# Performance work log

Hardware: AMD Instinct MI355X
Metric: run time of the kernel (lower is better)

The kernel has to match this reference:

```python
import jax, jax.numpy as jnp
import numpy as np
import math

DIM = 384
NH = 6
DH = DIM // NH
B = 2
S = 2048
EPS = 1e-6
LN_EPS = 1e-5


def setup_inputs() -> dict:
    key = jax.random.key(0)
    ks = jax.random.split(key, 8)
    q = jax.random.normal(ks[0], (B, S, DIM), dtype=jnp.float32)
    k = jax.random.normal(ks[1], (B, S, DIM), dtype=jnp.float32)
    v = jax.random.normal(ks[2], (B, S, DIM), dtype=jnp.float32)
    # gate linear params (Linear(3*dim, num_heads)); small random weights to exercise the math
    igate_w = jax.random.normal(ks[3], (NH, 3 * DIM), dtype=jnp.float32) * 0.02
    igate_b = jax.random.normal(ks[4], (NH,), dtype=jnp.float32) * 0.1
    fgate_w = jax.random.normal(ks[5], (NH, 3 * DIM), dtype=jnp.float32) * 0.02
    fgate_b = jnp.linspace(3.0, 6.0, NH, dtype=jnp.float32)
    # MultiHeadLayerNorm residual weight (stored as delta, effective scale = 1 + w)
    outnorm_weight = jax.random.normal(ks[6], (DIM,), dtype=jnp.float32) * 0.02
    return {"q": q, "k": k, "v": v, "igate_w": igate_w, "igate_b": igate_b,
            "fgate_w": fgate_w, "fgate_b": fgate_b, "outnorm_weight": outnorm_weight}


def _mlstm_forward(q, k, v, igate_w, igate_b, fgate_w, fgate_b, outnorm_weight):
    Bq, Sq, _ = q.shape
    gate_in = jnp.concatenate([q, k, v], axis=-1)                       # (B,S,3D)
    ig = gate_in @ igate_w.T + igate_b                                   # (B,S,NH)
    fg = gate_in @ fgate_w.T + fgate_b                                   # (B,S,NH)
    # split heads: (B,NH,S,DH)
    qh = q.reshape(Bq, Sq, NH, DH).transpose(0, 2, 1, 3)
    kh = k.reshape(Bq, Sq, NH, DH).transpose(0, 2, 1, 3)
    vh = v.reshape(Bq, Sq, NH, DH).transpose(0, 2, 1, 3)
    ig = ig.transpose(0, 2, 1)                                           # (B,NH,S)
    fg = fg.transpose(0, 2, 1)                                           # (B,NH,S)

    log_fg = jax.nn.log_sigmoid(fg)                                      # (B,NH,S)
    lfc = jnp.concatenate([jnp.zeros((Bq, NH, 1), dtype=q.dtype),
                           jnp.cumsum(log_fg, axis=-1)], axis=-1)        # (B,NH,S+1)
    # log_fg_matrix[i,j] = cumsum[i] - cumsum[j] (sliced [1:,1:]), masked causal
    diff = lfc[:, :, 1:, None] - lfc[:, :, None, 1:]                     # (B,NH,S,S)
    ltr = jnp.tril(jnp.ones((Sq, Sq), dtype=bool))
    log_fg_mat = jnp.where(ltr, diff, -jnp.inf)
    log_D = log_fg_mat + ig[:, :, None, :]                               # + igate^T
    max_log_D = jnp.max(log_D, axis=-1, keepdims=True)                   # rowwise stabilize
    D = jnp.exp(log_D - max_log_D)
    qk = jnp.einsum('bhsd,bhtd->bhst', qh, kh) / math.sqrt(DH)
    C = qk * D
    normalizer = jnp.maximum(jnp.abs(jnp.sum(C, axis=-1, keepdims=True)),
                             jnp.exp(-max_log_D))
    h = jnp.einsum('bhst,bhtd->bhsd', C / (normalizer + EPS), vh)        # (B,NH,S,DH)

    # MultiHeadLayerNorm == group_norm over each head's DH channels, scale=(1+w)
    mean = jnp.mean(h, axis=-1, keepdims=True)
    var = jnp.var(h, axis=-1, keepdims=True)
    normed = (h - mean) / jnp.sqrt(var + LN_EPS)
    scale = (1.0 + outnorm_weight).reshape(NH, DH)[None, :, None, :]
    out = normed * scale
    return out.transpose(0, 2, 1, 3).reshape(Bq, Sq, DIM)


def reference(q, k, v, igate_w, igate_b, fgate_w, fgate_b, outnorm_weight):
    return _mlstm_forward(q, k, v, igate_w, igate_b, fgate_w, fgate_b, outnorm_weight)
```

## Files before the change

### kernel.cpp

```cpp
#include <hip/hip_runtime.h>
#include <math.h>

#define DIM 384
#define NH 6
#define DH 64
#define B_ 2
#define S_ 2048
#define EPS 1e-6f
#define LN_EPS 1e-5f
#define G3 (3*DIM)
#define LOG2E 1.44269504f
#define KSTR 72
#define VSTR 68
#define NT (S_/64)
#define NSPLIT 8
#define NBH (B_*NH)

typedef __attribute__((ext_vector_type(8))) short bf16x8;
typedef __attribute__((ext_vector_type(4))) short bf16x4;
typedef __attribute__((ext_vector_type(4))) float f32x4;

__device__ __forceinline__ unsigned short f2bf(float f){
    unsigned int u = __float_as_uint(f);
    u += 0x7fff + ((u >> 16) & 1);
    return (unsigned short)(u >> 16);
}
__device__ __forceinline__ float bf2f(unsigned short u){
    return __uint_as_float(((unsigned int)u) << 16);
}

__device__ __forceinline__ float logsig(float x){
    return fminf(x, 0.f) - log1pf(expf(-fabsf(x)));
}

__global__ __launch_bounds__(256) void gates_kernel(
    const float* __restrict__ q, const float* __restrict__ k, const float* __restrict__ v,
    const float* __restrict__ iw, const float* __restrict__ ib,
    const float* __restrict__ fw, const float* __restrict__ fb,
    float* __restrict__ ig_out, float* __restrict__ lf_out) {
    int wave = (blockIdx.x * 256 + threadIdx.x) >> 6;
    int lane = threadIdx.x & 63;
    int b = wave / S_, s = wave % S_;
    size_t base = ((size_t)b * S_ + s) * DIM;
    float aI[NH], aF[NH];
    #pragma unroll
    for (int h = 0; h < NH; h++){ aI[h] = 0.f; aF[h] = 0.f; }
    for (int g = lane; g < G3/4; g += 64) {
        int e = g * 4;
        float4 x4;
        if (e < DIM)        x4 = *(const float4*)(q + base + e);
        else if (e < 2*DIM) x4 = *(const float4*)(k + base + e - DIM);
        else                x4 = *(const float4*)(v + base + e - 2*DIM);
        #pragma unroll
        for (int h = 0; h < NH; h++){
            float4 wi = *(const float4*)(iw + h*G3 + e);
            float4 wf = *(const float4*)(fw + h*G3 + e);
            aI[h] = fmaf(x4.x, wi.x, fmaf(x4.y, wi.y, fmaf(x4.z, wi.z, fmaf(x4.w, wi.w, aI[h]))));
            aF[h] = fmaf(x4.x, wf.x, fmaf(x4.y, wf.y, fmaf(x4.z, wf.z, fmaf(x4.w, wf.w, aF[h]))));
        }
    }
    #pragma unroll
    for (int h = 0; h < NH; h++){
        #pragma unroll
        for (int off = 32; off >= 1; off >>= 1){
            aI[h] += __shfl_xor(aI[h], off, 64);
            aF[h] += __shfl_xor(aF[h], off, 64);
        }
    }
    if (lane == 0) {
        #pragma unroll
        for (int h = 0; h < NH; h++){
            ig_out[((size_t)b*NH + h)*S_ + s] = aI[h] + ib[h];
            lf_out[((size_t)b*NH + h)*S_ + s] = logsig(aF[h] + fb[h]);
        }
    }
}

__global__ __launch_bounds__(256) void scan_kernel(const float* __restrict__ lf,
                                                   float* __restrict__ cum){
    int bh = blockIdx.x;
    const float* src = lf + (size_t)bh * S_;
    float* dst = cum + (size_t)bh * S_;
    int tid = threadIdx.x;
    float loc[8];
    float run = 0.f;
    #pragma unroll
    for (int j = 0; j < 8; j++){ run += src[tid*8 + j]; loc[j] = run; }
    __shared__ float sm[256];
    sm[tid] = run;
    __syncthreads();
    float total = run;
    for (int off = 1; off < 256; off <<= 1){
        float vv = (tid >= off) ? sm[tid - off] : 0.f;
        __syncthreads();
        sm[tid] += vv;
        __syncthreads();
    }
    float excl = sm[tid] - total;
    #pragma unroll
    for (int j = 0; j < 8; j++) dst[tid*8 + j] = excl + loc[j];
}

__global__ __launch_bounds__(256) void mlstm_part(
    const float* __restrict__ q, const float* __restrict__ k, const float* __restrict__ v,
    const float* __restrict__ ig, const float* __restrict__ cum,
    unsigned short* __restrict__ pOb, float* __restrict__ pM, float* __restrict__ pL) {
    int lin = blockIdx.x;
    int sp  = lin / NBH;
    int bh  = lin % NBH;
    int st  = (NT - 1) - (sp >> 3);
    int c   = sp & 7;
    int L   = (st + 8) >> 3;
    int tb0 = c * L;
    int tb1 = min((c + 1) * L, st + 1);
    int pblk = lin;
    int tid = threadIdx.x;

    if (tb0 >= tb1){
        if (tid < 64){ pM[pblk*64 + tid] = -INFINITY; pL[pblk*64 + tid] = 0.f; }
        return;
    }

    __shared__ unsigned short kt[64*KSTR];
    __shared__ unsigned short vt[64*VSTR];

    int b = bh / NH, h = bh % NH;
    int s0 = st * 64;
    int wv   = tid >> 6;
    int lane = tid & 63;
    int lq   = lane & 15;
    int quad = lane >> 4;

    const float* qbase = q + (size_t)b*S_*DIM + h*DH;
    const float* kbase = k + (size_t)b*S_*DIM + h*DH;
    const float* vbase = v + (size_t)b*S_*DIM + h*DH;
    const float* igb = ig + (size_t)bh*S_;
    const float* cmb = cum + (size_t)bh*S_;

    int s_glob = s0 + 16*wv + lq;

    bf16x8 qf[2];
    {
        const float* qr = qbase + (size_t)s_glob*DIM;
        #pragma unroll
        for (int ks = 0; ks < 2; ks++){
            float4 a = *(const float4*)(qr + 32*ks + 8*quad);
            float4 cc = *(const float4*)(qr + 32*ks + 8*quad + 4);
            bf16x8 t;
            t[0]=(short)f2bf(a.x*0.125f); t[1]=(short)f2bf(a.y*0.125f);
            t[2]=(short)f2bf(a.z*0.125f); t[3]=(short)f2bf(a.w*0.125f);
            t[4]=(short)f2bf(cc.x*0.125f); t[5]=(short)f2bf(cc.y*0.125f);
            t[6]=(short)f2bf(cc.z*0.125f); t[7]=(short)f2bf(cc.w*0.125f);
            qf[ks] = t;
        }
    }

    float cq  = cmb[s_glob];
    float m_s = -INFINITY, b_s = 0.f;
    f32x4 oacc[4];
    #pragma unroll
    for (int cg = 0; cg < 4; cg++) oacc[cg] = (f32x4){0.f,0.f,0.f,0.f};

    int srow[4], scol[4];
    #pragma unroll
    for (int i = 0; i < 4; i++){
        int idx = tid + 256*i;
        srow[i] = idx >> 4;
        scol[i] = (idx & 15) << 2;
    }

    float4 kreg[4], vreg[4];
    {
        const float* kb = kbase + (size_t)(tb0*64)*DIM;
        const float* vb = vbase + (size_t)(tb0*64)*DIM;
        #pragma unroll
        for (int i = 0; i < 4; i++){
            kreg[i] = *(const float4*)(kb + (size_t)srow[i]*DIM + scol[i]);
            vreg[i] = *(const float4*)(vb + (size_t)srow[i]*DIM + scol[i]);
        }
    }

    for (int t0 = tb0*64; t0 < tb1*64; t0 += 64){
        float4 cumc[4], igc[4];
        #pragma unroll
        for (int tb = 0; tb < 4; tb++){
            cumc[tb] = *(const float4*)(cmb + t0 + 16*tb + 4*quad);
            igc[tb]  = *(const float4*)(igb + t0 + 16*tb + 4*quad);
        }

        __syncthreads();
        #pragma unroll
        for (int i = 0; i < 4; i++){
            int r = srow[i], cc = scol[i];
            ushort4 kk; kk.x=f2bf(kreg[i].x); kk.y=f2bf(kreg[i].y);
            kk.z=f2bf(kreg[i].z); kk.w=f2bf(kreg[i].w);
            *(ushort4*)&kt[r*KSTR + cc] = kk;
            vt[(cc+0)*VSTR + r] = f2bf(vreg[i].x);
            vt[(cc+1)*VSTR + r] = f2bf(vreg[i].y);
            vt[(cc+2)*VSTR + r] = f2bf(vreg[i].z);
            vt[(cc+3)*VSTR + r] = f2bf(vreg[i].w);
        }
        __syncthreads();

        if (t0 + 64 < tb1*64){
            const float* kb = kbase + (size_t)(t0 + 64)*DIM;
            const float* vb = vbase + (size_t)(t0 + 64)*DIM;
            #pragma unroll
            for (int i = 0; i < 4; i++){
                kreg[i] = *(const float4*)(kb + (size_t)srow[i]*DIM + scol[i]);
                vreg[i] = *(const float4*)(vb + (size_t)srow[i]*DIM + scol[i]);
            }
        }

        f32x4 st4[4];
        #pragma unroll
        for (int tb = 0; tb < 4; tb++) st4[tb] = (f32x4){0.f,0.f,0.f,0.f};
        #pragma unroll
        for (int ks = 0; ks < 2; ks++){
            #pragma unroll
            for (int tb = 0; tb < 4; tb++){
                bf16x8 af = *(const bf16x8*)&kt[(16*tb + lq)*KSTR + 32*ks + 8*quad];
                st4[tb] = __builtin_amdgcn_mfma_f32_16x16x32_bf16(af, qf[ks], st4[tb], 0, 0, 0);
            }
        }

        bool diag = (t0 == s0);
        float dv[4][4];
        float pmax = -INFINITY;
        #pragma unroll
        for (int tb = 0; tb < 4; tb++){
            #pragma unroll
            for (int r = 0; r < 4; r++){
                float d = cq - cumc[tb][r] + igc[tb][r];
                if (diag && (t0 + 16*tb + 4*quad + r) > s_glob) d = -INFINITY;
                dv[tb][r] = d;
                pmax = fmaxf(pmax, d);
            }
        }
        pmax = fmaxf(pmax, __shfl_xor(pmax, 16, 64));
        pmax = fmaxf(pmax, __shfl_xor(pmax, 32, 64));
        float mn = fmaxf(m_s, pmax);
        float sc = exp2f((m_s - mn) * LOG2E);
        m_s = mn;
        float rs = 0.f;
        bf16x4 pf[4];
        #pragma unroll
        for (int tb = 0; tb < 4; tb++){
            #pragma unroll
            for (int r = 0; r < 4; r++){
                float pv = st4[tb][r] * exp2f((dv[tb][r] - mn) * LOG2E);
                rs += pv;
                pf[tb][r] = (short)f2bf(pv);
            }
        }
        rs += __shfl_xor(rs, 16, 64);
        rs += __shfl_xor(rs, 32, 64);
        b_s = b_s * sc + rs;

        #pragma unroll
        for (int r = 0; r < 4; r++){
            float sco = __shfl(sc, 20*quad + r, 64);
            #pragma unroll
            for (int cg = 0; cg < 4; cg++) oacc[cg][r] *= sco;
        }

        #pragma unroll
        for (int tb = 0; tb < 4; tb++){
            #pragma unroll
            for (int cg = 0; cg < 4; cg++){
                bf16x4 vf = *(const bf16x4*)&vt[(16*cg + lq)*VSTR + 16*tb + 4*quad];
                oacc[cg] = __builtin_amdgcn_mfma_f32_16x16x16bf16_1k(pf[tb], vf, oacc[cg], 0, 0, 0);
            }
        }
    }

    unsigned short* po = pOb + (size_t)pblk * 4096;
    #pragma unroll
    for (int r = 0; r < 4; r++){
        int row = 16*wv + 4*quad + r;
        #pragma unroll
        for (int cg = 0; cg < 4; cg++)
            po[row*64 + 16*cg + lq] = f2bf(oacc[cg][r]);
    }
    if (quad == 0){
        pM[pblk*64 + 16*wv + lq] = m_s;
        pL[pblk*64 + 16*wv + lq] = b_s;
    }
}

__global__ __launch_bounds__(256) void mlstm_combine(
    const unsigned short* __restrict__ pOb, const float* __restrict__ pM,
    const float* __restrict__ pL, const float* __restrict__ w,
    float* __restrict__ out) {
    int st = blockIdx.x;
    int bh = blockIdx.y;
    int b = bh / NH, h = bh % NH;
    int tid = threadIdx.x;
    int cl = (tid & 15) * 4;
    int rb = tid >> 4;

    int pblk[NSPLIT];
    #pragma unroll
    for (int p = 0; p < NSPLIT; p++)
        pblk[p] = (((NT - 1 - st) << 3) + p) * NBH + bh;

    float4 wv4 = *(const float4*)(w + h*DH + cl);

    #pragma unroll
    for (int pass = 0; pass < 4; pass++){
        int row = pass*16 + rb;
        float mp[NSPLIT], lp[NSPLIT];
        float mmax = -INFINITY;
        #pragma unroll
        for (int p = 0; p < NSPLIT; p++){
            mp[p] = pM[pblk[p]*64 + row];
            lp[p] = pL[pblk[p]*64 + row];
            mmax = fmaxf(mmax, mp[p]);
        }
        float l = 0.f;
        float ox = 0.f, oy = 0.f, oz = 0.f, ow = 0.f;
        #pragma unroll
        for (int p = 0; p < NSPLIT; p++){
            if (mp[p] != -INFINITY){
                float wp = exp2f((mp[p] - mmax) * LOG2E);
                l += wp * lp[p];
                ushort4 t4 = *(const ushort4*)(pOb + (size_t)pblk[p]*4096 + row*64 + cl);
                ox += wp*bf2f(t4.x); oy += wp*bf2f(t4.y);
                oz += wp*bf2f(t4.z); ow += wp*bf2f(t4.w);
            }
        }
        float nrm = fmaxf(fabsf(l), exp2f(-mmax * LOG2E));
        float inv = 1.f / (nrm + EPS);
        float x[4] = {ox*inv, oy*inv, oz*inv, ow*inv};
        float s1 = x[0]+x[1]+x[2]+x[3];
        float s2 = x[0]*x[0]+x[1]*x[1]+x[2]*x[2]+x[3]*x[3];
        #pragma unroll
        for (int off = 8; off >= 1; off >>= 1){
            s1 += __shfl_xor(s1, off, 64);
            s2 += __shfl_xor(s2, off, 64);
        }
        float mean = s1 * (1.f/64.f);
        float var  = s2 * (1.f/64.f) - mean*mean;
        float rstd = rsqrtf(var + LN_EPS);
        float4 oo;
        oo.x = (x[0]-mean)*rstd*(1.f + wv4.x);
        oo.y = (x[1]-mean)*rstd*(1.f + wv4.y);
        oo.z = (x[2]-mean)*rstd*(1.f + wv4.z);
        oo.w = (x[3]-mean)*rstd*(1.f + wv4.w);
        *(float4*)(out + ((size_t)b*S_ + st*64 + row)*DIM + h*DH + cl) = oo;
    }
}

extern "C" void kernel_launch(void* const* d_in, const int* in_sizes, int n_in,
                              void* d_out, int out_size, void* d_ws, size_t ws_size,
                              hipStream_t stream) {
    const float* q  = (const float*)d_in[0];
    const float* k  = (const float*)d_in[1];
    const float* v  = (const float*)d_in[2];
    const float* iw = (const float*)d_in[3];
    const float* ib = (const float*)d_in[4];
    const float* fw = (const float*)d_in[5];
    const float* fb = (const float*)d_in[6];
    const float* w  = (const float*)d_in[7];
    float* out = (float*)d_out;

    const int nPart = NBH * NT * NSPLIT;
    float* ig  = (float*)d_ws;
    float* lf  = ig  + (size_t)NBH*S_;
    float* cum = lf  + (size_t)NBH*S_;
    float* pM  = cum + (size_t)NBH*S_;
    float* pL  = pM  + (size_t)nPart*64;
    unsigned short* pOb = (unsigned short*)(pL + (size_t)nPart*64);

    gates_kernel<<<B_*S_/4, 256, 0, stream>>>(q, k, v, iw, ib, fw, fb, ig, lf);
    scan_kernel<<<NBH, 256, 0, stream>>>(lf, cum);
    mlstm_part<<<nPart, 256, 0, stream>>>(q, k, v, ig, cum, pOb, pM, pL);
    mlstm_combine<<<dim3(NT, NBH), 256, 0, stream>>>(pOb, pM, pL, w, out);
}
```

Measured before the change: 157.3 us.

## Pre-convert Q/K to bf16 and V to transposed bf16 once; halve KV split count

Adds two pre-pass kernels that turn Q (pre-scaled) and K into bf16, and V into a per-head transposed bf16 layout, all stored in workspace. The attention part kernel then loads bf16 tiles directly with 16-byte vector copies into LDS, so it no longer repeats the fp32-to-bf16 conversion and scattered transpose stores for every tile. The KV split factor drops from 8 to 4, which means fewer partial outputs to write and combine but less parallelism per query tile. This costs two extra launches and an extra pass over Q, K and V in memory.

```diff
diff --git a/kernel.cpp b/kernel.cpp
--- a/kernel.cpp
+++ b/kernel.cpp
@@ -11,14 +11,14 @@
 #define G3 (3*DIM)
 #define LOG2E 1.44269504f
 #define KSTR 72
-#define VSTR 68
 #define NT (S_/64)
-#define NSPLIT 8
+#define NSPLIT 4
 #define NBH (B_*NH)
 
 typedef __attribute__((ext_vector_type(8))) short bf16x8;
 typedef __attribute__((ext_vector_type(4))) short bf16x4;
 typedef __attribute__((ext_vector_type(4))) float f32x4;
+typedef __attribute__((ext_vector_type(8))) unsigned short u16x8;
 
 __device__ __forceinline__ unsigned short f2bf(float f){
     unsigned int u = __float_as_uint(f);
@@ -28,9 +28,55 @@
 __device__ __forceinline__ float bf2f(unsigned short u){
     return __uint_as_float(((unsigned int)u) << 16);
 }
-
 __device__ __forceinline__ float logsig(float x){
     return fminf(x, 0.f) - log1pf(expf(-fabsf(x)));
+}
+
+__global__ __launch_bounds__(256) void cvtqk_kernel(
+    const float* __restrict__ q, const float* __restrict__ k,
+    unsigned short* __restrict__ Qb, unsigned short* __restrict__ Kb) {
+    size_t base = ((size_t)blockIdx.x * 256 + threadIdx.x) * 8;
+    float4 a = *(const float4*)(q + base);
+    float4 b = *(const float4*)(q + base + 4);
+    u16x8 t;
+    t[0]=f2bf(a.x*0.125f); t[1]=f2bf(a.y*0.125f); t[2]=f2bf(a.z*0.125f); t[3]=f2bf(a.w*0.125f);
+    t[4]=f2bf(b.x*0.125f); t[5]=f2bf(b.y*0.125f); t[6]=f2bf(b.z*0.125f); t[7]=f2bf(b.w*0.125f);
+    *(u16x8*)(Qb + base) = t;
+    float4 c = *(const float4*)(k + base);
+    float4 d = *(const float4*)(k + base + 4);
+    u16x8 s;
+    s[0]=f2bf(c.x); s[1]=f2bf(c.y); s[2]=f2bf(c.z); s[3]=f2bf(c.w);
+    s[4]=f2bf(d.x); s[5]=f2bf(d.y); s[6]=f2bf(d.z); s[7]=f2bf(d.w);
+    *(u16x8*)(Kb + base) = s;
+}
+
+__global__ __launch_bounds__(256) void cvtv_kernel(
+    const float* __restrict__ v, unsigned short* __restrict__ Vt) {
+    __shared__ unsigned short lt[64*KSTR];
+    int bh = blockIdx.y;
+    int b = bh / NH, h = bh % NH;
+    int t0 = blockIdx.x * 64;
+    int tid = threadIdx.x;
+    #pragma unroll
+    for (int i = 0; i < 4; i++){
+        int idx = tid + 256*i;
+        int r = idx >> 4;
+        int c4 = (idx & 15) * 4;
+        float4 x = *(const float4*)(v + ((size_t)b*S_ + t0 + r)*DIM + h*DH + c4);
+        lt[(c4+0)*KSTR + r] = f2bf(x.x);
+        lt[(c4+1)*KSTR + r] = f2bf(x.y);
+        lt[(c4+2)*KSTR + r] = f2bf(x.z);
+        lt[(c4+3)*KSTR + r] = f2bf(x.w);
+    }
+    __syncthreads();
+    #pragma unroll
+    for (int i = 0; i < 2; i++){
+        int idx = tid + 256*i;
+        int d = idx >> 3;
+        int t8 = (idx & 7) * 8;
+        u16x8 o = *(const u16x8*)&lt[d*KSTR + t8];
+        *(u16x8*)(Vt + (size_t)bh*DH*S_ + (size_t)d*S_ + t0 + t8) = o;
+    }
 }
 
 __global__ __launch_bounds__(256) void gates_kernel(
@@ -102,15 +148,16 @@
 }
 
 __global__ __launch_bounds__(256) void mlstm_part(
-    const float* __restrict__ q, const float* __restrict__ k, const float* __restrict__ v,
+    const unsigned short* __restrict__ Qb, const unsigned short* __restrict__ Kb,
+    const unsigned short* __restrict__ Vt,
     const float* __restrict__ ig, const float* __restrict__ cum,
     unsigned short* __restrict__ pOb, float* __restrict__ pM, float* __restrict__ pL) {
     int lin = blockIdx.x;
     int sp  = lin / NBH;
     int bh  = lin % NBH;
-    int st  = (NT - 1) - (sp >> 3);
-    int c   = sp & 7;
-    int L   = (st + 8) >> 3;
+    int st  = (NT - 1) - (sp >> 2);
+    int c   = sp & 3;
+    int L   = (st + 4) >> 2;
     int tb0 = c * L;
     int tb1 = min((c + 1) * L, st + 1);
     int pblk = lin;
@@ -122,7 +169,7 @@
     }
 
     __shared__ unsigned short kt[64*KSTR];
-    __shared__ unsigned short vt[64*VSTR];
+    __shared__ unsigned short vt[64*KSTR];
 
     int b = bh / NH, h = bh % NH;
     int s0 = st * 64;
@@ -131,9 +178,8 @@
     int lq   = lane & 15;
     int quad = lane >> 4;
 
-    const float* qbase = q + (size_t)b*S_*DIM + h*DH;
-    const float* kbase = k + (size_t)b*S_*DIM + h*DH;
-    const float* vbase = v + (size_t)b*S_*DIM + h*DH;
+    const unsigned short* kbT = Kb + (size_t)b*S_*DIM + h*DH;
+    const unsigned short* vtB = Vt + (size_t)bh*DH*S_;
     const float* igb = ig + (size_t)bh*S_;
     const float* cmb = cum + (size_t)bh*S_;
 
@@ -141,18 +187,9 @@
 
     bf16x8 qf[2];
     {
-        const float* qr = qbase + (size_t)s_glob*DIM;
-        #pragma unroll
-        for (int ks = 0; ks < 2; ks++){
-            float4 a = *(const float4*)(qr + 32*ks + 8*quad);
-            float4 cc = *(const float4*)(qr + 32*ks + 8*quad + 4);
-            bf16x8 t;
-            t[0]=(short)f2bf(a.x*0.125f); t[1]=(short)f2bf(a.y*0.125f);
-            t[2]=(short)f2bf(a.z*0.125f); t[3]=(short)f2bf(a.w*0.125f);
-            t[4]=(short)f2bf(cc.x*0.125f); t[5]=(short)f2bf(cc.y*0.125f);
-            t[6]=(short)f2bf(cc.z*0.125f); t[7]=(short)f2bf(cc.w*0.125f);
-            qf[ks] = t;
-        }
+        const unsigned short* qr = Qb + ((size_t)b*S_ + s_glob)*DIM + h*DH;
+        qf[0] = *(const bf16x8*)(qr + 8*quad);
+        qf[1] = *(const bf16x8*)(qr + 32 + 8*quad);
     }
 
     float cq  = cmb[s_glob];
@@ -161,22 +198,22 @@
     #pragma unroll
     for (int cg = 0; cg < 4; cg++) oacc[cg] = (f32x4){0.f,0.f,0.f,0.f};
 
-    int srow[4], scol[4];
-    #pragma unroll
-    for (int i = 0; i < 4; i++){
+    int sr[2], sc[2];
+    #pragma unroll
+    for (int i = 0; i < 2; i++){
         int idx = tid + 256*i;
-        srow[i] = idx >> 4;
-        scol[i] = (idx & 15) << 2;
-    }
-
-    float4 kreg[4], vreg[4];
+        sr[i] = idx >> 3;
+        sc[i] = (idx & 7) * 8;
+    }
+
+    u16x8 kreg[2], vreg[2];
     {
-        const float* kb = kbase + (size_t)(tb0*64)*DIM;
-        const float* vb = vbase + (size_t)(tb0*64)*DIM;
-        #pragma unroll
-        for (int i = 0; i < 4; i++){
-            kreg[i] = *(const float4*)(kb + (size_t)srow[i]*DIM + scol[i]);
-            vreg[i] = *(const float4*)(vb + (size_t)srow[i]*DIM + scol[i]);
+        const unsigned short* kb = kbT + (size_t)(tb0*64)*DIM;
+        const unsigned short* vb = vtB + tb0*64;
+        #pragma unroll
+        for (int i = 0; i < 2; i++){
+            kreg[i] = *(const u16x8*)(kb + (size_t)sr[i]*DIM + sc[i]);
+            vreg[i] = *(const u16x8*)(vb + (size_t)sr[i]*S_ + sc[i]);
         }
     }
 
@@ -190,25 +227,19 @@
 
         __syncthreads();
         #pragma unroll
-        for (int i = 0; i < 4; i++){
-            int r = srow[i], cc = scol[i];
-            ushort4 kk; kk.x=f2bf(kreg[i].x); kk.y=f2bf(kreg[i].y);
-            kk.z=f2bf(kreg[i].z); kk.w=f2bf(kreg[i].w);
-            *(ushort4*)&kt[r*KSTR + cc] = kk;
-            vt[(cc+0)*VSTR + r] = f2bf(vreg[i].x);
-            vt[(cc+1)*VSTR + r] = f2bf(vreg[i].y);
-            vt[(cc+2)*VSTR + r] = f2bf(vreg[i].z);
-            vt[(cc+3)*VSTR + r] = f2bf(vreg[i].w);
+        for (int i = 0; i < 2; i++){
+            *(u16x8*)&kt[sr[i]*KSTR + sc[i]] = kreg[i];
+            *(u16x8*)&vt[sr[i]*KSTR + sc[i]] = vreg[i];
         }
         __syncthreads();
 
         if (t0 + 64 < tb1*64){
-            const float* kb = kbase + (size_t)(t0 + 64)*DIM;
-            const float* vb = vbase + (size_t)(t0 + 64)*DIM;
-            #pragma unroll
-            for (int i = 0; i < 4; i++){
-                kreg[i] = *(const float4*)(kb + (size_t)srow[i]*DIM + scol[i]);
-                vreg[i] = *(const float4*)(vb + (size_t)srow[i]*DIM + scol[i]);
+            const unsigned short* kb = kbT + (size_t)(t0 + 64)*DIM;
+            const unsigned short* vb = vtB + (t0 + 64);
+            #pragma unroll
+            for (int i = 0; i < 2; i++){
+                kreg[i] = *(const u16x8*)(kb + (size_t)sr[i]*DIM + sc[i]);
+                vreg[i] = *(const u16x8*)(vb + (size_t)sr[i]*S_ + sc[i]);
             }
         }
 
@@ -240,7 +271,7 @@
         pmax = fmaxf(pmax, __shfl_xor(pmax, 16, 64));
         pmax = fmaxf(pmax, __shfl_xor(pmax, 32, 64));
         float mn = fmaxf(m_s, pmax);
-        float sc = exp2f((m_s - mn) * LOG2E);
+        float sc2 = exp2f((m_s - mn) * LOG2E);
         m_s = mn;
         float rs = 0.f;
         bf16x4 pf[4];
@@ -255,11 +286,11 @@
         }
         rs += __shfl_xor(rs, 16, 64);
         rs += __shfl_xor(rs, 32, 64);
-        b_s = b_s * sc + rs;
+        b_s = b_s * sc2 + rs;
 
         #pragma unroll
         for (int r = 0; r < 4; r++){
-            float sco = __shfl(sc, 20*quad + r, 64);
+            float sco = __shfl(sc2, 20*quad + r, 64);
             #pragma unroll
             for (int cg = 0; cg < 4; cg++) oacc[cg][r] *= sco;
         }
@@ -268,7 +299,7 @@
         for (int tb = 0; tb < 4; tb++){
             #pragma unroll
             for (int cg = 0; cg < 4; cg++){
-                bf16x4 vf = *(const bf16x4*)&vt[(16*cg + lq)*VSTR + 16*tb + 4*quad];
+                bf16x4 vf = *(const bf16x4*)&vt[(16*cg + lq)*KSTR + 16*tb + 4*quad];
                 oacc[cg] = __builtin_amdgcn_mfma_f32_16x16x16bf16_1k(pf[tb], vf, oacc[cg], 0, 0, 0);
             }
         }
@@ -302,7 +333,7 @@
     int pblk[NSPLIT];
     #pragma unroll
     for (int p = 0; p < NSPLIT; p++)
-        pblk[p] = (((NT - 1 - st) << 3) + p) * NBH + bh;
+        pblk[p] = (((NT - 1 - st) << 2) + p) * NBH + bh;
 
     float4 wv4 = *(const float4*)(w + h*DH + cl);
 
@@ -365,15 +396,21 @@
     float* out = (float*)d_out;
 
     const int nPart = NBH * NT * NSPLIT;
+    const size_t NE = (size_t)B_ * S_ * DIM;
     float* ig  = (float*)d_ws;
     float* lf  = ig  + (size_t)NBH*S_;
     float* cum = lf  + (size_t)NBH*S_;
     float* pM  = cum + (size_t)NBH*S_;
     float* pL  = pM  + (size_t)nPart*64;
     unsigned short* pOb = (unsigned short*)(pL + (size_t)nPart*64);
-
+    unsigned short* Qb  = pOb + (size_t)nPart*4096;
+    unsigned short* Kb  = Qb + NE;
+    unsigned short* Vt  = Kb + NE;
+
+    cvtqk_kernel<<<NE/8/256, 256, 0, stream>>>(q, k, Qb, Kb);
+    cvtv_kernel<<<dim3(NT, NBH), 256, 0, stream>>>(v, Vt);
     gates_kernel<<<B_*S_/4, 256, 0, stream>>>(q, k, v, iw, ib, fw, fb, ig, lf);
     scan_kernel<<<NBH, 256, 0, stream>>>(lf, cum);
-    mlstm_part<<<nPart, 256, 0, stream>>>(q, k, v, ig, cum, pOb, pM, pL);
+    mlstm_part<<<nPart, 256, 0, stream>>>(Qb, Kb, Vt, ig, cum, pOb, pM, pL);
     mlstm_combine<<<dim3(NT, NBH), 256, 0, stream>>>(pOb, pM, pL, w, out);
 }
```

Result: faster. 142.0 us (-9.7%).
